# Kernel tuning notes

Measured on AMD Instinct MI355X. Metric: run time of the kernel, lower is better.

## Reference

```python
import jax, jax.numpy as jnp
import numpy as np

B, S, H, F, E, K = 4, 2048, 2048, 8192, 8, 2  # batch, seq, hidden, d_ff, num_experts, topk


def setup_inputs() -> dict:
    key = jax.random.key(0)
    k0, k1, k2, k3 = jax.random.split(key, 4)
    x = jax.random.normal(k0, (B, S, H), dtype=jnp.float32)
    Wr = jax.random.normal(k1, (H, E), dtype=jnp.float32) * 0.02   # router weight
    br = jnp.zeros((E,), dtype=jnp.float32)
    W1 = jax.random.normal(k2, (E, H, F), dtype=jnp.float32) * 0.02  # per-expert up-proj
    b1 = jnp.zeros((E, F), dtype=jnp.float32)
    W2 = jax.random.normal(k3, (E, F, H), dtype=jnp.float32) * 0.02  # per-expert down-proj
    b2 = jnp.zeros((E, H), dtype=jnp.float32)
    return {"x": x, "Wr": Wr, "br": br, "W1": W1, "b1": b1, "W2": W2, "b2": b2}


def reference(x, Wr, br, W1, b1, W2, b2):
    b, s, h = x.shape
    xt = x.reshape(b * s, h)                      # (N, H), N = b*s
    logits = xt @ Wr + br                         # (N, E) router
    gates = jax.nn.softmax(logits, axis=-1)
    G, idx = jax.lax.top_k(gates, K)              # (N, K), (N, K)
    P = jax.nn.one_hot(idx, E, dtype=xt.dtype)    # (N, K, E) dispatch one-hot
    # tokens_for_expert: einsum('nk,nh->kh', P[...,e], x) for each expert -> (E, K, H)
    tok = jnp.einsum('nke,nh->ekh', P, xt)
    # per-expert FFN (exact GELU, matching torch nn.GELU default)
    mid = jax.nn.gelu(jnp.einsum('ekh,ehf->ekf', tok, W1) + b1[:, None, :], approximate=False)
    Eo = jnp.einsum('ekf,efh->ekh', mid, W2) + b2[:, None, :]   # (E, K, H)
    # combine: sum_e einsum('nk,kh->nh', G, E_e)
    y = jnp.einsum('nk,ekh->nh', G, Eo)
    return y.reshape(b, s, h)
```

## Files before the change

### kernel.cpp

```cpp
#include <hip/hip_runtime.h>
#include <math.h>

#define NTOK 8192
#define HDIM 2048
#define FDIM 8192
#define NEXP 8

typedef float f32x4 __attribute__((ext_vector_type(4)));

__global__ __launch_bounds__(256) void router_kernel(const float* __restrict__ x,
                                                     const float* __restrict__ Wr,
                                                     const float* __restrict__ br,
                                                     const float* __restrict__ b2,
                                                     float* __restrict__ G,
                                                     int* __restrict__ sel,
                                                     float* __restrict__ tok,
                                                     float* __restrict__ ebar) {
  {
    const int idx = blockIdx.x * 256 + threadIdx.x;
    if (idx < (16 * HDIM) / 4) {
      *(float4*)(tok + idx * 4) = make_float4(0.f, 0.f, 0.f, 0.f);
    } else if (idx < (16 * HDIM) / 4 + 1024) {
      const int j = idx - (16 * HDIM) / 4;
      const int h = (j & 511) << 2;
      float4 s = make_float4(0.f, 0.f, 0.f, 0.f);
#pragma unroll
      for (int e = 0; e < 8; ++e) {
        float4 b = *(const float4*)(b2 + e * HDIM + h);
        s.x += b.x; s.y += b.y; s.z += b.z; s.w += b.w;
      }
      *(float4*)(ebar + (j >> 9) * HDIM + h) = s;
    }
  }
  const int wave = threadIdx.x >> 6;
  const int lane = threadIdx.x & 63;
  const int n0 = (blockIdx.x * 4 + wave) * 4;

  float acc[4][8];
#pragma unroll
  for (int t = 0; t < 4; ++t)
#pragma unroll
    for (int e = 0; e < 8; ++e) acc[t][e] = 0.f;

#pragma unroll 4
  for (int j = 0; j < 32; ++j) {
    const int h = lane + (j << 6);
    float4 wa = *(const float4*)(Wr + h * 8);
    float4 wb = *(const float4*)(Wr + h * 8 + 4);
    float w[8] = {wa.x, wa.y, wa.z, wa.w, wb.x, wb.y, wb.z, wb.w};
#pragma unroll
    for (int t = 0; t < 4; ++t) {
      float xv = x[(size_t)(n0 + t) * HDIM + h];
#pragma unroll
      for (int e = 0; e < 8; ++e) acc[t][e] = fmaf(xv, w[e], acc[t][e]);
    }
  }

#pragma unroll
  for (int t = 0; t < 4; ++t)
#pragma unroll
    for (int e = 0; e < 8; ++e) {
      float v = acc[t][e];
      v += __shfl_xor(v, 1, 64);
      v += __shfl_xor(v, 2, 64);
      v += __shfl_xor(v, 4, 64);
      v += __shfl_xor(v, 8, 64);
      v += __shfl_xor(v, 16, 64);
      v += __shfl_xor(v, 32, 64);
      acc[t][e] = v;
    }

  if (lane == 0) {
    float brv[8];
#pragma unroll
    for (int e = 0; e < 8; ++e) brv[e] = br[e];
#pragma unroll
    for (int t = 0; t < 4; ++t) {
      float l[8];
#pragma unroll
      for (int e = 0; e < 8; ++e) l[e] = acc[t][e] + brv[e];
      float m = l[0];
#pragma unroll
      for (int e = 1; e < 8; ++e) m = fmaxf(m, l[e]);
      float s = 0.f;
#pragma unroll
      for (int e = 0; e < 8; ++e) s += expf(l[e] - m);
      float best = l[0], second = -3.4e38f;
      int bi = 0, si = 0;
#pragma unroll
      for (int e = 1; e < 8; ++e) {
        float v = l[e];
        if (v > best) { second = best; si = bi; best = v; bi = e; }
        else if (v > second) { second = v; si = e; }
      }
      const int n = n0 + t;
      const float inv = 1.f / s;
      G[n * 2 + 0] = expf(best - m) * inv;
      G[n * 2 + 1] = expf(second - m) * inv;
      sel[n * 2 + 0] = bi;
      sel[n * 2 + 1] = si;
    }
  }
}

__global__ __launch_bounds__(256) void tok_kernel(const float* __restrict__ x,
                                                  const int* __restrict__ sel,
                                                  float* __restrict__ tok) {
  __shared__ float2 part[16][256];
  __shared__ int sidx[256];
  const int tid = threadIdx.x;
  const int h0 = blockIdx.x << 9;
  const int n0 = blockIdx.y << 7;
#pragma unroll
  for (int s = 0; s < 16; ++s) part[s][tid] = make_float2(0.f, 0.f);
  sidx[tid] = sel[(n0 << 1) + tid];
  __syncthreads();
#pragma unroll 8
  for (int i = 0; i < 128; ++i) {
    float2 v = *(const float2*)(x + (size_t)(n0 + i) * HDIM + h0 + tid * 2);
    int s0 = sidx[2 * i] << 1;
    int s1 = (sidx[2 * i + 1] << 1) + 1;
    part[s0][tid].x += v.x; part[s0][tid].y += v.y;
    part[s1][tid].x += v.x; part[s1][tid].y += v.y;
  }
#pragma unroll
  for (int s = 0; s < 16; ++s) {
    atomicAdd(&tok[s * HDIM + h0 + tid * 2 + 0], part[s][tid].x);
    atomicAdd(&tok[s * HDIM + h0 + tid * 2 + 1], part[s][tid].y);
  }
}

__global__ __launch_bounds__(256) void up_kernel(const float* __restrict__ tok,
                                                 const float* __restrict__ W1,
                                                 float* __restrict__ up_part) {
  const int e = blockIdx.y;
  const int hc = blockIdx.x;
  const int tid = threadIdx.x;
  const int h0 = hc << 5;
  __shared__ float ts[2][32];
  if (tid < 32)       ts[0][tid] = tok[(e * 2 + 0) * HDIM + h0 + tid];
  else if (tid < 64)  ts[1][tid - 32] = tok[(e * 2 + 1) * HDIM + h0 + (tid - 32)];
  __syncthreads();

  float4 a0[8], a1[8];
#pragma unroll
  for (int j = 0; j < 8; ++j) {
    a0[j] = make_float4(0.f, 0.f, 0.f, 0.f);
    a1[j] = make_float4(0.f, 0.f, 0.f, 0.f);
  }
  const float* base = W1 + ((size_t)e * HDIM + h0) * FDIM;
#pragma unroll 2
  for (int h = 0; h < 32; ++h) {
    const float* row = base + (size_t)h * FDIM;
    const float t0 = ts[0][h], t1 = ts[1][h];
#pragma unroll
    for (int j = 0; j < 8; ++j) {
      f32x4 w = __builtin_nontemporal_load(
          reinterpret_cast<const f32x4*>(row + ((j << 8) + tid) * 4));
      a0[j].x = fmaf(t0, w.x, a0[j].x); a0[j].y = fmaf(t0, w.y, a0[j].y);
      a0[j].z = fmaf(t0, w.z, a0[j].z); a0[j].w = fmaf(t0, w.w, a0[j].w);
      a1[j].x = fmaf(t1, w.x, a1[j].x); a1[j].y = fmaf(t1, w.y, a1[j].y);
      a1[j].z = fmaf(t1, w.z, a1[j].z); a1[j].w = fmaf(t1, w.w, a1[j].w);
    }
  }
  float* p0 = up_part + (size_t)((e * 64 + hc) * 2 + 0) * FDIM;
  float* p1 = up_part + (size_t)((e * 64 + hc) * 2 + 1) * FDIM;
#pragma unroll
  for (int j = 0; j < 8; ++j) {
    *(float4*)(p0 + ((j << 8) + tid) * 4) = a0[j];
    *(float4*)(p1 + ((j << 8) + tid) * 4) = a1[j];
  }
}

__global__ __launch_bounds__(256) void down_kernel(const float* __restrict__ up_part,
                                                   const float* __restrict__ b1,
                                                   const float* __restrict__ W2,
                                                   float* __restrict__ down_part) {
  const int e = blockIdx.y;
  const int fc = blockIdx.x;
  const int tid = threadIdx.x;
  const int f0 = fc << 7;
  __shared__ float ms[2][128];
  {
    const int k = tid >> 7;
    const int fl = tid & 127;
    float acc = 0.f;
#pragma unroll
    for (int hc = 0; hc < 64; ++hc)
      acc += up_part[(size_t)((e * 64 + hc) * 2 + k) * FDIM + f0 + fl];
    acc += b1[e * FDIM + f0 + fl];
    ms[k][fl] = 0.5f * acc * (1.f + erff(acc * 0.70710678118654752f));
  }
  __syncthreads();

  float4 a[2][2];
#pragma unroll
  for (int k = 0; k < 2; ++k)
#pragma unroll
    for (int j = 0; j < 2; ++j) a[k][j] = make_float4(0.f, 0.f, 0.f, 0.f);
  const float* base = W2 + ((size_t)e * FDIM + f0) * HDIM;
#pragma unroll 8
  for (int ff = 0; ff < 128; ++ff) {
    const float* row = base + (size_t)ff * HDIM;
    const float m0 = ms[0][ff], m1 = ms[1][ff];
#pragma unroll
    for (int j = 0; j < 2; ++j) {
      f32x4 w = __builtin_nontemporal_load(
          reinterpret_cast<const f32x4*>(row + ((j << 8) + tid) * 4));
      a[0][j].x = fmaf(m0, w.x, a[0][j].x); a[0][j].y = fmaf(m0, w.y, a[0][j].y);
      a[0][j].z = fmaf(m0, w.z, a[0][j].z); a[0][j].w = fmaf(m0, w.w, a[0][j].w);
      a[1][j].x = fmaf(m1, w.x, a[1][j].x); a[1][j].y = fmaf(m1, w.y, a[1][j].y);
      a[1][j].z = fmaf(m1, w.z, a[1][j].z); a[1][j].w = fmaf(m1, w.w, a[1][j].w);
    }
  }
#pragma unroll
  for (int k = 0; k < 2; ++k) {
    float* p = down_part + (size_t)((e * 64 + fc) * 2 + k) * HDIM;
#pragma unroll
    for (int j = 0; j < 2; ++j) *(float4*)(p + ((j << 8) + tid) * 4) = a[k][j];
  }
}

__global__ __launch_bounds__(256) void ebar_reduce_kernel(const float* __restrict__ down_part,
                                                          float* __restrict__ ebar) {
  const int tid = threadIdx.x;
  const int c0 = blockIdx.x * 8;
  float4 acc[2][2];
#pragma unroll
  for (int k = 0; k < 2; ++k)
#pragma unroll
    for (int r = 0; r < 2; ++r) acc[k][r] = make_float4(0.f, 0.f, 0.f, 0.f);
#pragma unroll
  for (int j = 0; j < 8; ++j) {
    const int c = c0 + j;
#pragma unroll
    for (int k = 0; k < 2; ++k) {
      const float* base = down_part + (size_t)(c * 2 + k) * HDIM;
#pragma unroll
      for (int r = 0; r < 2; ++r) {
        float4 v = *(const float4*)(base + ((r << 8) + tid) * 4);
        acc[k][r].x += v.x; acc[k][r].y += v.y; acc[k][r].z += v.z; acc[k][r].w += v.w;
      }
    }
  }
#pragma unroll
  for (int k = 0; k < 2; ++k)
#pragma unroll
    for (int r = 0; r < 2; ++r) {
      float* dst = ebar + k * HDIM + ((r << 8) + tid) * 4;
      atomicAdd(dst + 0, acc[k][r].x);
      atomicAdd(dst + 1, acc[k][r].y);
      atomicAdd(dst + 2, acc[k][r].z);
      atomicAdd(dst + 3, acc[k][r].w);
    }
}

__global__ __launch_bounds__(256) void combine_kernel(const float* __restrict__ G,
                                                      const float* __restrict__ ebar,
                                                      float* __restrict__ y) {
  const int i4 = blockIdx.x * 256 + threadIdx.x;
  const int n = i4 >> 9;
  const int h = (i4 & 511) << 2;
  const float g0 = G[n * 2 + 0], g1 = G[n * 2 + 1];
  float4 e0 = *(const float4*)(ebar + h);
  float4 e1 = *(const float4*)(ebar + HDIM + h);
  f32x4 r;
  r.x = fmaf(g0, e0.x, g1 * e1.x);
  r.y = fmaf(g0, e0.y, g1 * e1.y);
  r.z = fmaf(g0, e0.z, g1 * e1.z);
  r.w = fmaf(g0, e0.w, g1 * e1.w);
  __builtin_nontemporal_store(r, reinterpret_cast<f32x4*>(y + ((size_t)n << 11) + h));
}

extern "C" void kernel_launch(void* const* d_in, const int* in_sizes, int n_in,
                              void* d_out, int out_size, void* d_ws, size_t ws_size,
                              hipStream_t stream) {
  const float* x  = (const float*)d_in[0];
  const float* Wr = (const float*)d_in[1];
  const float* br = (const float*)d_in[2];
  const float* W1 = (const float*)d_in[3];
  const float* b1 = (const float*)d_in[4];
  const float* W2 = (const float*)d_in[5];
  const float* b2 = (const float*)d_in[6];
  float* y = (float*)d_out;

  char* ws = (char*)d_ws;
  float* G         = (float*)(ws);
  int*   sel       = (int*)(ws + (64 << 10));
  float* tok       = (float*)(ws + (128 << 10));
  float* ebar      = (float*)(ws + (256 << 10));
  float* up_part   = (float*)(ws + (512 << 10));
  float* down_part = (float*)(ws + (512 << 10) + (32 << 20));

  router_kernel<<<512, 256, 0, stream>>>(x, Wr, br, b2, G, sel, tok, ebar);
  tok_kernel<<<dim3(4, 64), 256, 0, stream>>>(x, sel, tok);
  up_kernel<<<dim3(64, 8), 256, 0, stream>>>(tok, W1, up_part);
  down_kernel<<<dim3(64, 8), 256, 0, stream>>>(up_part, b1, W2, down_part);
  ebar_reduce_kernel<<<64, 256, 0, stream>>>(down_part, ebar);
  combine_kernel<<<16384, 256, 0, stream>>>(G, ebar, y);
}
```

Measured before the change: 258.7 us.

## Split GEMV grids for more blocks and hoist GELU reduction into separate kernel

```diff
diff --git a/kernel.cpp b/kernel.cpp
--- a/kernel.cpp
+++ b/kernel.cpp
@@ -106,55 +106,54 @@
 __global__ __launch_bounds__(256) void tok_kernel(const float* __restrict__ x,
                                                   const int* __restrict__ sel,
                                                   float* __restrict__ tok) {
-  __shared__ float2 part[16][256];
+  __shared__ float part[16][256];
   __shared__ int sidx[256];
   const int tid = threadIdx.x;
-  const int h0 = blockIdx.x << 9;
+  const int h0 = blockIdx.x << 8;
   const int n0 = blockIdx.y << 7;
 #pragma unroll
-  for (int s = 0; s < 16; ++s) part[s][tid] = make_float2(0.f, 0.f);
+  for (int s = 0; s < 16; ++s) part[s][tid] = 0.f;
   sidx[tid] = sel[(n0 << 1) + tid];
   __syncthreads();
 #pragma unroll 8
   for (int i = 0; i < 128; ++i) {
-    float2 v = *(const float2*)(x + (size_t)(n0 + i) * HDIM + h0 + tid * 2);
+    float v = x[(size_t)(n0 + i) * HDIM + h0 + tid];
     int s0 = sidx[2 * i] << 1;
     int s1 = (sidx[2 * i + 1] << 1) + 1;
-    part[s0][tid].x += v.x; part[s0][tid].y += v.y;
-    part[s1][tid].x += v.x; part[s1][tid].y += v.y;
-  }
-#pragma unroll
-  for (int s = 0; s < 16; ++s) {
-    atomicAdd(&tok[s * HDIM + h0 + tid * 2 + 0], part[s][tid].x);
-    atomicAdd(&tok[s * HDIM + h0 + tid * 2 + 1], part[s][tid].y);
-  }
+    part[s0][tid] += v;
+    part[s1][tid] += v;
+  }
+#pragma unroll
+  for (int s = 0; s < 16; ++s) atomicAdd(&tok[s * HDIM + h0 + tid], part[s][tid]);
 }
 
 __global__ __launch_bounds__(256) void up_kernel(const float* __restrict__ tok,
                                                  const float* __restrict__ W1,
                                                  float* __restrict__ up_part) {
-  const int e = blockIdx.y;
+  const int e = blockIdx.z;
+  const int fh = blockIdx.y;
   const int hc = blockIdx.x;
   const int tid = threadIdx.x;
   const int h0 = hc << 5;
+  const int fbase = fh << 12;
   __shared__ float ts[2][32];
   if (tid < 32)       ts[0][tid] = tok[(e * 2 + 0) * HDIM + h0 + tid];
   else if (tid < 64)  ts[1][tid - 32] = tok[(e * 2 + 1) * HDIM + h0 + (tid - 32)];
   __syncthreads();
 
-  float4 a0[8], a1[8];
-#pragma unroll
-  for (int j = 0; j < 8; ++j) {
+  float4 a0[4], a1[4];
+#pragma unroll
+  for (int j = 0; j < 4; ++j) {
     a0[j] = make_float4(0.f, 0.f, 0.f, 0.f);
     a1[j] = make_float4(0.f, 0.f, 0.f, 0.f);
   }
-  const float* base = W1 + ((size_t)e * HDIM + h0) * FDIM;
+  const float* base = W1 + ((size_t)e * HDIM + h0) * FDIM + fbase;
 #pragma unroll 2
   for (int h = 0; h < 32; ++h) {
     const float* row = base + (size_t)h * FDIM;
     const float t0 = ts[0][h], t1 = ts[1][h];
 #pragma unroll
-    for (int j = 0; j < 8; ++j) {
+    for (int j = 0; j < 4; ++j) {
       f32x4 w = __builtin_nontemporal_load(
           reinterpret_cast<const f32x4*>(row + ((j << 8) + tid) * 4));
       a0[j].x = fmaf(t0, w.x, a0[j].x); a0[j].y = fmaf(t0, w.y, a0[j].y);
@@ -163,62 +162,68 @@
       a1[j].z = fmaf(t1, w.z, a1[j].z); a1[j].w = fmaf(t1, w.w, a1[j].w);
     }
   }
-  float* p0 = up_part + (size_t)((e * 64 + hc) * 2 + 0) * FDIM;
-  float* p1 = up_part + (size_t)((e * 64 + hc) * 2 + 1) * FDIM;
-#pragma unroll
-  for (int j = 0; j < 8; ++j) {
+  float* p0 = up_part + (size_t)((e * 64 + hc) * 2 + 0) * FDIM + fbase;
+  float* p1 = up_part + (size_t)((e * 64 + hc) * 2 + 1) * FDIM + fbase;
+#pragma unroll
+  for (int j = 0; j < 4; ++j) {
     *(float4*)(p0 + ((j << 8) + tid) * 4) = a0[j];
     *(float4*)(p1 + ((j << 8) + tid) * 4) = a1[j];
   }
 }
 
-__global__ __launch_bounds__(256) void down_kernel(const float* __restrict__ up_part,
-                                                   const float* __restrict__ b1,
+__global__ __launch_bounds__(128) void gelu_reduce_kernel(const float* __restrict__ up_part,
+                                                          const float* __restrict__ b1,
+                                                          float* __restrict__ mid) {
+  const int i4 = blockIdx.x * 128 + threadIdx.x;
+  const int f = (i4 & (FDIM / 4 - 1)) << 2;
+  const int ek = i4 >> 11;
+  const int e = ek >> 1;
+  float4 s = make_float4(0.f, 0.f, 0.f, 0.f);
+#pragma unroll 16
+  for (int hc = 0; hc < 64; ++hc) {
+    float4 v = *(const float4*)(up_part + (size_t)((e * 64 + hc) * 2 + (ek & 1)) * FDIM + f);
+    s.x += v.x; s.y += v.y; s.z += v.z; s.w += v.w;
+  }
+  float4 b = *(const float4*)(b1 + e * FDIM + f);
+  s.x += b.x; s.y += b.y; s.z += b.z; s.w += b.w;
+  float4 r;
+  r.x = 0.5f * s.x * (1.f + erff(s.x * 0.70710678118654752f));
+  r.y = 0.5f * s.y * (1.f + erff(s.y * 0.70710678118654752f));
+  r.z = 0.5f * s.z * (1.f + erff(s.z * 0.70710678118654752f));
+  r.w = 0.5f * s.w * (1.f + erff(s.w * 0.70710678118654752f));
+  *(float4*)(mid + (size_t)ek * FDIM + f) = r;
+}
+
+__global__ __launch_bounds__(256) void down_kernel(const float* __restrict__ mid,
                                                    const float* __restrict__ W2,
                                                    float* __restrict__ down_part) {
-  const int e = blockIdx.y;
+  const int e = blockIdx.z;
+  const int hh = blockIdx.y;
   const int fc = blockIdx.x;
   const int tid = threadIdx.x;
   const int f0 = fc << 7;
+  const int hbase = hh << 10;
   __shared__ float ms[2][128];
-  {
-    const int k = tid >> 7;
-    const int fl = tid & 127;
-    float acc = 0.f;
-#pragma unroll
-    for (int hc = 0; hc < 64; ++hc)
-      acc += up_part[(size_t)((e * 64 + hc) * 2 + k) * FDIM + f0 + fl];
-    acc += b1[e * FDIM + f0 + fl];
-    ms[k][fl] = 0.5f * acc * (1.f + erff(acc * 0.70710678118654752f));
-  }
+  if (tid < 128) ms[0][tid] = mid[(e * 2 + 0) * FDIM + f0 + tid];
+  else           ms[1][tid - 128] = mid[(e * 2 + 1) * FDIM + f0 + (tid - 128)];
   __syncthreads();
 
-  float4 a[2][2];
-#pragma unroll
-  for (int k = 0; k < 2; ++k)
-#pragma unroll
-    for (int j = 0; j < 2; ++j) a[k][j] = make_float4(0.f, 0.f, 0.f, 0.f);
-  const float* base = W2 + ((size_t)e * FDIM + f0) * HDIM;
+  float4 a0 = make_float4(0.f, 0.f, 0.f, 0.f), a1 = make_float4(0.f, 0.f, 0.f, 0.f);
+  const float* base = W2 + ((size_t)e * FDIM + f0) * HDIM + hbase + tid * 4;
 #pragma unroll 8
   for (int ff = 0; ff < 128; ++ff) {
-    const float* row = base + (size_t)ff * HDIM;
+    f32x4 w = __builtin_nontemporal_load(
+        reinterpret_cast<const f32x4*>(base + (size_t)ff * HDIM));
     const float m0 = ms[0][ff], m1 = ms[1][ff];
-#pragma unroll
-    for (int j = 0; j < 2; ++j) {
-      f32x4 w = __builtin_nontemporal_load(
-          reinterpret_cast<const f32x4*>(row + ((j << 8) + tid) * 4));
-      a[0][j].x = fmaf(m0, w.x, a[0][j].x); a[0][j].y = fmaf(m0, w.y, a[0][j].y);
-      a[0][j].z = fmaf(m0, w.z, a[0][j].z); a[0][j].w = fmaf(m0, w.w, a[0][j].w);
-      a[1][j].x = fmaf(m1, w.x, a[1][j].x); a[1][j].y = fmaf(m1, w.y, a[1][j].y);
-      a[1][j].z = fmaf(m1, w.z, a[1][j].z); a[1][j].w = fmaf(m1, w.w, a[1][j].w);
-    }
-  }
-#pragma unroll
-  for (int k = 0; k < 2; ++k) {
-    float* p = down_part + (size_t)((e * 64 + fc) * 2 + k) * HDIM;
-#pragma unroll
-    for (int j = 0; j < 2; ++j) *(float4*)(p + ((j << 8) + tid) * 4) = a[k][j];
-  }
+    a0.x = fmaf(m0, w.x, a0.x); a0.y = fmaf(m0, w.y, a0.y);
+    a0.z = fmaf(m0, w.z, a0.z); a0.w = fmaf(m0, w.w, a0.w);
+    a1.x = fmaf(m1, w.x, a1.x); a1.y = fmaf(m1, w.y, a1.y);
+    a1.z = fmaf(m1, w.z, a1.z); a1.w = fmaf(m1, w.w, a1.w);
+  }
+  float* p0 = down_part + (size_t)((e * 64 + fc) * 2 + 0) * HDIM + hbase + tid * 4;
+  float* p1 = down_part + (size_t)((e * 64 + fc) * 2 + 1) * HDIM + hbase + tid * 4;
+  *(float4*)p0 = a0;
+  *(float4*)p1 = a1;
 }
 
 __global__ __launch_bounds__(256) void ebar_reduce_kernel(const float* __restrict__ down_part,
@@ -289,13 +294,15 @@
   int*   sel       = (int*)(ws + (64 << 10));
   float* tok       = (float*)(ws + (128 << 10));
   float* ebar      = (float*)(ws + (256 << 10));
-  float* up_part   = (float*)(ws + (512 << 10));
-  float* down_part = (float*)(ws + (512 << 10) + (32 << 20));
+  float* mid       = (float*)(ws + (320 << 10));
+  float* up_part   = (float*)(ws + (1 << 20));
+  float* down_part = (float*)(ws + (1 << 20) + (32 << 20));
 
   router_kernel<<<512, 256, 0, stream>>>(x, Wr, br, b2, G, sel, tok, ebar);
-  tok_kernel<<<dim3(4, 64), 256, 0, stream>>>(x, sel, tok);
-  up_kernel<<<dim3(64, 8), 256, 0, stream>>>(tok, W1, up_part);
-  down_kernel<<<dim3(64, 8), 256, 0, stream>>>(up_part, b1, W2, down_part);
+  tok_kernel<<<dim3(8, 64), 256, 0, stream>>>(x, sel, tok);
+  up_kernel<<<dim3(64, 2, 8), 256, 0, stream>>>(tok, W1, up_part);
+  gelu_reduce_kernel<<<256, 128, 0, stream>>>(up_part, b1, mid);
+  down_kernel<<<dim3(64, 2, 8), 256, 0, stream>>>(mid, W2, down_part);
   ebar_reduce_kernel<<<64, 256, 0, stream>>>(down_part, ebar);
   combine_kernel<<<16384, 256, 0, stream>>>(G, ebar, y);
 }
```

Result: faster. 251.2 us (-2.9%).
